# Kernel tuning notes

Measured on AMD Instinct MI355X. Metric: run time of the kernel, lower is better.

Reference implementation:

```python
import jax, jax.numpy as jnp
import numpy as np

N_NODES = 50000
N_EDGES = 600000
LATENT = 128
STEPS = 4
BN_EPS = 1e-5


def _bn(h, gamma, beta):
    # BatchNorm1d in training mode: batch statistics over the row dim (biased var)
    mean = jnp.mean(h, axis=0)
    var = jnp.var(h, axis=0)
    return gamma * (h - mean) * jax.lax.rsqrt(var + BN_EPS) + beta


def setup_inputs() -> dict:
    key = jax.random.key(0)
    ks = jax.random.split(key, 9)
    L, S = LATENT, STEPS
    d = {}
    d["x"] = jax.random.normal(ks[0], (N_NODES, L), dtype=jnp.float32)
    d["edge_attr"] = jax.random.normal(ks[1], (N_EDGES, L), dtype=jnp.float32)
    d["edge_index"] = jax.random.randint(ks[2], (2, N_EDGES), 0, N_NODES, dtype=jnp.int64)
    # MLP weights: small init (BN normalizes hidden activations anyway)
    d["edge_W1"] = jax.random.normal(ks[3], (S, 3 * L, L), dtype=jnp.float32) * (1.0 / np.sqrt(3 * L))
    d["edge_b1"] = jnp.zeros((S, L), jnp.float32)
    d["edge_g1"] = jnp.ones((S, L), jnp.float32)
    d["edge_be1"] = jnp.zeros((S, L), jnp.float32)
    d["edge_W2"] = jax.random.normal(ks[4], (S, L, L), dtype=jnp.float32) * (1.0 / np.sqrt(L))
    d["edge_b2"] = jnp.zeros((S, L), jnp.float32)
    d["node_W1"] = jax.random.normal(ks[5], (S, 2 * L, L), dtype=jnp.float32) * (1.0 / np.sqrt(2 * L))
    d["node_b1"] = jnp.zeros((S, L), jnp.float32)
    d["node_g1"] = jnp.ones((S, L), jnp.float32)
    d["node_be1"] = jnp.zeros((S, L), jnp.float32)
    d["node_W2"] = jax.random.normal(ks[6], (S, L, L), dtype=jnp.float32) * (1.0 / np.sqrt(L))
    d["node_b2"] = jnp.zeros((S, L), jnp.float32)
    return d


def reference(x, edge_attr, edge_index, edge_W1, edge_b1, edge_g1, edge_be1,
              edge_W2, edge_b2, node_W1, node_b1, node_g1, node_be1,
              node_W2, node_b2):
    src = edge_index[0]  # x_j (source)
    dst = edge_index[1]  # x_i (target), also the scatter target
    for s in range(STEPS):
        # --- edge update (message) ---
        m = jnp.concatenate([x[dst], x[src], edge_attr], axis=1)  # [E, 3L]
        h = _bn(m @ edge_W1[s] + edge_b1[s], edge_g1[s], edge_be1[s])
        h = jax.nn.relu(h)
        h = jax.nn.relu(h @ edge_W2[s] + edge_b2[s])
        edge_attr = h + edge_attr  # residual
        # --- aggregate: scatter-sum to target nodes ---
        agg = jax.ops.segment_sum(edge_attr, dst, num_segments=N_NODES)  # [N, L]
        # --- node update ---
        n = jnp.concatenate([x, agg], axis=1)  # [N, 2L]
        h = _bn(n @ node_W1[s] + node_b1[s], node_g1[s], node_be1[s])
        h = jax.nn.relu(h)
        h = jax.nn.relu(h @ node_W2[s] + node_b2[s])
        x = h + x  # residual
    return x, edge_attr
```

## Files before the change

kernel.cpp:

```cpp
#include <hip/hip_runtime.h>
#include <hip/hip_bf16.h>
#include <cstdint>
#include <cstddef>

#define E_N 600000
#define NND 50000
#define L 128
#define EGRID 4688
#define PBLK 16384

typedef unsigned short u16;
typedef unsigned int u32;
typedef __attribute__((ext_vector_type(8))) short bf16x8;
typedef __attribute__((ext_vector_type(4))) float f32x4;

static __device__ __forceinline__ u16 f2bf(float f) {
  union { float f; u32 u; } c; c.f = f;
  return (u16)((c.u + 0x7fffu + ((c.u >> 16) & 1u)) >> 16);
}
static __device__ __forceinline__ u32 pk2(float a, float b) {
  return (u32)f2bf(a) | ((u32)f2bf(b) << 16);
}
static __device__ __forceinline__ float bf2f(u32 h) {
  union { u32 u; float f; } c; c.u = (h & 0xffffu) << 16; return c.f;
}
static __device__ __forceinline__ void atomAddF(float* p, float v) {
#if defined(__HIP_DEVICE_COMPILE__)
  unsafeAtomicAdd(p, v);
#else
  atomicAdd(p, v);
#endif
}
static __device__ __forceinline__ bf16x8 bnrelu8(bf16x8 raw, float4 sca, float4 scb,
                                                 float4 sha, float4 shb) {
  union { bf16x8 v; u16 h[8]; } in; in.v = raw;
  const float sc[8] = {sca.x, sca.y, sca.z, sca.w, scb.x, scb.y, scb.z, scb.w};
  const float sh[8] = {sha.x, sha.y, sha.z, sha.w, shb.x, shb.y, shb.z, shb.w};
  float f[8];
  #pragma unroll
  for (int i = 0; i < 8; ++i) f[i] = fmaxf(bf2f(in.h[i]) * sc[i] + sh[i], 0.f);
  union { bf16x8 v; u32 w[4]; } r;
  #pragma unroll
  for (int i = 0; i < 4; ++i) r.w[i] = pk2(f[2 * i], f[2 * i + 1]);
  return r.v;
}

#define MFMA(a, bfr, c) __builtin_amdgcn_mfma_f32_16x16x32_bf16((a), (bfr), (c), 0, 0, 0)

static __device__ __forceinline__ size_t paddr(int row, int panel, int incol) {
  return (size_t)(row >> 7) * PBLK + (size_t)panel * 2048 + (size_t)(row & 127) * 16 + incol;
}

__global__ __launch_bounds__(256) void k_cvt4(const float* __restrict__ in,
                                              u16* __restrict__ out, int n4) {
  const int i = blockIdx.x * 256 + threadIdx.x;
  if (i < n4) {
    const float4 v = *(const float4*)(in + (size_t)i * 4);
    uint2 o; o.x = pk2(v.x, v.y); o.y = pk2(v.z, v.w);
    *(uint2*)(out + (size_t)i * 4) = o;
  }
}

__global__ __launch_bounds__(256) void k_cvtperm(const float* __restrict__ in_ea,
                                                 const int* __restrict__ perm,
                                                 u16* __restrict__ ea16) {
  const int i = blockIdx.x * 256 + threadIdx.x;
  const int row = i >> 4, part = i & 15;
  if (row < E_N) {
    const float* p = in_ea + (size_t)perm[row] * L + part * 8;
    const float4 f0 = *(const float4*)p, f1 = *(const float4*)(p + 4);
    union { bf16x8 v; u32 w[4]; } r;
    r.w[0] = pk2(f0.x, f0.y); r.w[1] = pk2(f0.z, f0.w);
    r.w[2] = pk2(f1.x, f1.y); r.w[3] = pk2(f1.z, f1.w);
    *(bf16x8*)(ea16 + paddr(row, part >> 1, (part & 1) * 8)) = r.v;
  }
}

__global__ void k_wt(const float* __restrict__ W, u16* __restrict__ Wt, int K) {
  const int idx = blockIdx.x * 256 + threadIdx.x;
  const int total = 4 * K * 128;
  if (idx >= total) return;
  const int s = idx / (K * 128);
  const int rem = idx - s * K * 128;
  const int n = rem / K;
  const int k = rem - n * K;
  Wt[idx] = f2bf(W[(size_t)s * K * 128 + (size_t)k * 128 + n]);
}

__global__ void k_hist(const int* __restrict__ dstI, int* __restrict__ cnt) {
  const int i = blockIdx.x * 256 + threadIdx.x;
  if (i < E_N) atomicAdd(&cnt[dstI[i]], 1);
}

__global__ __launch_bounds__(1024) void k_scan(const int* __restrict__ cnt, int* __restrict__ startA) {
  __shared__ int buf[1024];
  __shared__ int carry;
  const int tid = threadIdx.x;
  if (tid == 0) carry = 0;
  __syncthreads();
  for (int base = 0; base < NND; base += 1024) {
    int v = (base + tid < NND) ? cnt[base + tid] : 0;
    buf[tid] = v;
    __syncthreads();
    for (int off = 1; off < 1024; off <<= 1) {
      int t = (tid >= off) ? buf[tid - off] : 0;
      __syncthreads();
      buf[tid] += t;
      __syncthreads();
    }
    const int incl = buf[tid];
    const int c = carry;
    if (base + tid < NND) startA[base + tid] = c + incl - v;
    __syncthreads();
    if (tid == 1023) carry = c + incl;
    __syncthreads();
  }
  if (tid == 0) startA[NND] = carry;
}

__global__ void k_fill(const int* __restrict__ dstI, const int* __restrict__ startA,
                       int* __restrict__ cur, int* __restrict__ eids) {
  const int i = blockIdx.x * 256 + threadIdx.x;
  if (i < E_N) {
    const int d = dstI[i];
    const int pos = atomicAdd(&cur[d], 1);
    eids[startA[d] + pos] = i;
  }
}

__global__ void k_perm(const int* __restrict__ srcI, const int* __restrict__ dstI,
                       const int* __restrict__ perm,
                       int* __restrict__ srcP, int* __restrict__ dstP) {
  const int i = blockIdx.x * 256 + threadIdx.x;
  if (i < E_N) {
    const int e = perm[i];
    srcP[i] = srcI[e];
    dstP[i] = dstI[e];
  }
}

__global__ __launch_bounds__(256) void k_agg(const u16* __restrict__ ea16,
                                             const int* __restrict__ startA,
                                             u16* __restrict__ agg16) {
  const int node = blockIdx.x * 4 + (threadIdx.x >> 6);
  const int lane = threadIdx.x & 63;
  if (node >= NND) return;
  const int s = startA[node], e = startA[node + 1];
  const size_t poff = (size_t)(lane >> 3) * 2048 + (size_t)((lane & 7) * 2);
  float a0 = 0.f, a1 = 0.f, b0 = 0.f, b1 = 0.f;
  int i = s;
  for (; i + 1 < e; i += 2) {
    const u32 v0 = *(const u32*)(ea16 + (size_t)(i >> 7) * PBLK + (size_t)(i & 127) * 16 + poff);
    const int j = i + 1;
    const u32 v1 = *(const u32*)(ea16 + (size_t)(j >> 7) * PBLK + (size_t)(j & 127) * 16 + poff);
    a0 += bf2f(v0); a1 += bf2f(v0 >> 16);
    b0 += bf2f(v1); b1 += bf2f(v1 >> 16);
  }
  if (i < e) {
    const u32 v = *(const u32*)(ea16 + (size_t)(i >> 7) * PBLK + (size_t)(i & 127) * 16 + poff);
    a0 += bf2f(v); a1 += bf2f(v >> 16);
  }
  *(u32*)(agg16 + (size_t)node * L + lane * 2) = pk2(a0 + b0, a1 + b1);
}

__global__ void k_bnfin(const float* __restrict__ gS, const float* __restrict__ g,
                        const float* __restrict__ be, float invM, float* __restrict__ ss) {
  const int c = threadIdx.x;
  float s1 = 0.f, s2 = 0.f;
  for (int j = 0; j < 64; ++j) { s1 += gS[j * L + c]; s2 += gS[64 * L + j * L + c]; }
  const float mean = s1 * invM;
  const float var = s2 * invM - mean * mean;
  const float sc = g[c] * rsqrtf(var + 1e-5f);
  ss[c] = sc;
  ss[L + c] = be[c] - mean * sc;
}

__global__ __launch_bounds__(512, 4) void k_edge_l1(
    const u16* __restrict__ x16, const u16* __restrict__ ea16,
    const int* __restrict__ srcP, const int* __restrict__ dstP,
    const u16* __restrict__ Wt, const float* __restrict__ b,
    u16* __restrict__ h1, float* __restrict__ gS)
{
  __shared__ __align__(16) char Ws2[2 * 16384];
  __shared__ float red[256];
  const int tid = threadIdx.x, bid = blockIdx.x, row0 = bid * 128;
  const int lane = tid & 63, wid = tid >> 6;
  const int wr = wid >> 1, wc = wid & 1;
  const int l15 = lane & 15, lq = lane >> 4;
  if (tid < 256) red[tid] = 0.f;

  int crw[2], dI[2], sI[2];
  #pragma unroll
  for (int m = 0; m < 2; ++m) {
    crw[m] = min(row0 + wr * 32 + m * 16 + l15, E_N - 1);
    dI[m] = dstP[crw[m]];
    sI[m] = srcP[crw[m]];
  }

  bf16x8 af3[3][2][2];
  auto loadA = [&](int cc, bf16x8 (&dst)[2][2]) {
    #pragma unroll
    for (int m = 0; m < 2; ++m) {
      if (cc < 4) {
        const int node = (cc < 2) ? dI[m] : sI[m];
        const u16* p = x16 + (size_t)node * L + (cc & 1) * 64 + lq * 8;
        dst[m][0] = *(const bf16x8*)p;
        dst[m][1] = *(const bf16x8*)(p + 32);
      } else {
        const int pc = cc - 4;
        dst[m][0] = *(const bf16x8*)(ea16 + paddr(crw[m], pc * 4 + (lq >> 1), (lq & 1) * 8));
        dst[m][1] = *(const bf16x8*)(ea16 + paddr(crw[m], pc * 4 + 2 + (lq >> 1), (lq & 1) * 8));
      }
    }
  };
  loadA(0, af3[0]); loadA(1, af3[1]); loadA(2, af3[2]);

  const int n0 = tid >> 3,         kq0 = (tid & 7) ^ (n0 & 7);
  const int n1 = (tid + 512) >> 3, kq1 = ((tid + 512) & 7) ^ (n1 & 7);
  uint4 wa, wb;
  auto wload = [&](int cc) {
    wa = *(const uint4*)(Wt + (size_t)n0 * 384 + cc * 64 + kq0 * 8);
    wb = *(const uint4*)(Wt + (size_t)n1 * 384 + cc * 64 + kq1 * 8);
  };
  auto wwrite = [&](int buf) {
    *(uint4*)(Ws2 + buf * 16384 + tid * 16) = wa;
    *(uint4*)(Ws2 + buf * 16384 + tid * 16 + 8192) = wb;
  };

  wload(0);
  wwrite(0);
  __syncthreads();

  f32x4 acc[2][4];
  #pragma unroll
  for (int m = 0; m < 2; ++m)
    #pragma unroll
    for (int n = 0; n < 4; ++n) acc[m][n] = (f32x4){0.f, 0.f, 0.f, 0.f};

  #pragma unroll
  for (int cc = 0; cc < 6; ++cc) {
    if (cc + 1 < 6) wload(cc + 1);
    const char* base = Ws2 + (cc & 1) * 16384;
    const bf16x8 (&af)[2][2] = af3[cc % 3];
    #pragma unroll
    for (int k2 = 0; k2 < 2; ++k2)
      #pragma unroll
      for (int n = 0; n < 4; ++n) {
        const int ncol = wc * 64 + n * 16 + l15;
        const int sw = (ncol & 7) << 4;
        const bf16x8 wf = *(const bf16x8*)(base + ((ncol * 128 + k2 * 64 + lq * 16) ^ sw));
        acc[0][n] = MFMA(wf, af[0][k2], acc[0][n]);
        acc[1][n] = MFMA(wf, af[1][k2], acc[1][n]);
      }
    if (cc + 3 < 6) loadA(cc + 3, af3[cc % 3]);
    if (cc + 1 < 6) wwrite((cc + 1) & 1);
    __syncthreads();
  }

  #pragma unroll
  for (int m = 0; m < 2; ++m) {
    const int rl = wr * 32 + m * 16 + l15;
    const bool valid = row0 + rl < E_N;
    #pragma unroll
    for (int n = 0; n < 4; ++n) {
      const int colb = wc * 64 + n * 16 + lq * 4;
      const float4 bb = *(const float4*)(b + colb);
      float o[4], s1[4], s2[4];
      o[0] = acc[m][n][0] + bb.x; o[1] = acc[m][n][1] + bb.y;
      o[2] = acc[m][n][2] + bb.z; o[3] = acc[m][n][3] + bb.w;
      #pragma unroll
      for (int r = 0; r < 4; ++r) {
        s1[r] = valid ? o[r] : 0.f;
        s2[r] = valid ? o[r] * o[r] : 0.f;
      }
      if (valid) {
        ushort4 st;
        st.x = f2bf(o[0]); st.y = f2bf(o[1]); st.z = f2bf(o[2]); st.w = f2bf(o[3]);
        *(ushort4*)(h1 + (size_t)bid * PBLK + (size_t)(wc * 4 + n) * 2048 + rl * 16 + lq * 4) = st;
      }
      #pragma unroll
      for (int off = 1; off < 16; off <<= 1)
        #pragma unroll
        for (int r = 0; r < 4; ++r) {
          s1[r] += __shfl_xor(s1[r], off);
          s2[r] += __shfl_xor(s2[r], off);
        }
      if (l15 == 0) {
        #pragma unroll
        for (int r = 0; r < 4; ++r) {
          atomAddF(&red[colb + r], s1[r]);
          atomAddF(&red[128 + colb + r], s2[r]);
        }
      }
    }
  }
  __syncthreads();
  const int slot = (bid & 63) * L;
  if (tid < 128) atomAddF(&gS[slot + tid], red[tid]);
  else if (tid < 256) atomAddF(&gS[64 * L + slot + (tid - 128)], red[tid]);
}

template <bool WF32>
__global__ __launch_bounds__(512, 4) void k_edge_l2(
    const u16* __restrict__ h1, const float* __restrict__ ss,
    const u16* __restrict__ Wt, const float* __restrict__ b,
    const int* __restrict__ perm,
    float* __restrict__ ea_out, u16* __restrict__ ea16)
{
  __shared__ __align__(16) char Ws2[2 * 16384];
  const int tid = threadIdx.x, bid = blockIdx.x, row0 = bid * 128;
  const int lane = tid & 63, wid = tid >> 6;
  const int wr = wid >> 1, wc = wid & 1;
  const int l15 = lane & 15, lq = lane >> 4;

  int crw[2];
  #pragma unroll
  for (int m = 0; m < 2; ++m)
    crw[m] = min(row0 + wr * 32 + m * 16 + l15, E_N - 1);

  const int n0 = tid >> 3,         kq0 = (tid & 7) ^ (n0 & 7);
  const int n1 = (tid + 512) >> 3, kq1 = ((tid + 512) & 7) ^ (n1 & 7);
  #pragma unroll
  for (int cc = 0; cc < 2; ++cc) {
    const uint4 wa = *(const uint4*)(Wt + (size_t)n0 * 128 + cc * 64 + kq0 * 8);
    const uint4 wb = *(const uint4*)(Wt + (size_t)n1 * 128 + cc * 64 + kq1 * 8);
    *(uint4*)(Ws2 + cc * 16384 + tid * 16) = wa;
    *(uint4*)(Ws2 + cc * 16384 + tid * 16 + 8192) = wb;
  }

  bf16x8 ah[2][2][2];
  #pragma unroll
  for (int cc = 0; cc < 2; ++cc)
    #pragma unroll
    for (int m = 0; m < 2; ++m)
      #pragma unroll
      for (int k2 = 0; k2 < 2; ++k2)
        ah[cc][m][k2] = *(const bf16x8*)(h1 + paddr(crw[m], cc * 4 + k2 * 2 + (lq >> 1), (lq & 1) * 8));
  __syncthreads();

  f32x4 acc[2][4];
  #pragma unroll
  for (int m = 0; m < 2; ++m)
    #pragma unroll
    for (int n = 0; n < 4; ++n) acc[m][n] = (f32x4){0.f, 0.f, 0.f, 0.f};

  #pragma unroll
  for (int cc = 0; cc < 2; ++cc)
    #pragma unroll
    for (int k2 = 0; k2 < 2; ++k2) {
      const int kb = cc * 64 + k2 * 32 + lq * 8;
      const float4 sca = *(const float4*)(ss + kb), scb = *(const float4*)(ss + kb + 4);
      const float4 sha = *(const float4*)(ss + 128 + kb), shb = *(const float4*)(ss + 128 + kb + 4);
      const bf16x8 a0 = bnrelu8(ah[cc][0][k2], sca, scb, sha, shb);
      const bf16x8 a1 = bnrelu8(ah[cc][1][k2], sca, scb, sha, shb);
      const char* base = Ws2 + cc * 16384;
      #pragma unroll
      for (int n = 0; n < 4; ++n) {
        const int ncol = wc * 64 + n * 16 + l15;
        const int sw = (ncol & 7) << 4;
        const bf16x8 wf = *(const bf16x8*)(base + ((ncol * 128 + k2 * 64 + lq * 16) ^ sw));
        acc[0][n] = MFMA(wf, a0, acc[0][n]);
        acc[1][n] = MFMA(wf, a1, acc[1][n]);
      }
    }

  #pragma unroll
  for (int m = 0; m < 2; ++m) {
    const int rl = wr * 32 + m * 16 + l15;
    const int row = row0 + rl;
    if (row < E_N) {
      const int prow = WF32 ? perm[row] : 0;
      #pragma unroll
      for (int n = 0; n < 4; ++n) {
        const int colb = wc * 64 + n * 16 + lq * 4;
        const float4 bb = *(const float4*)(b + colb);
        float o[4];
        o[0] = fmaxf(acc[m][n][0] + bb.x, 0.f);
        o[1] = fmaxf(acc[m][n][1] + bb.y, 0.f);
        o[2] = fmaxf(acc[m][n][2] + bb.z, 0.f);
        o[3] = fmaxf(acc[m][n][3] + bb.w, 0.f);
        u16* ep = ea16 + (size_t)bid * PBLK + (size_t)(wc * 4 + n) * 2048 + rl * 16 + lq * 4;
        const ushort4 rv = *(const ushort4*)ep;
        o[0] += bf2f(rv.x); o[1] += bf2f(rv.y); o[2] += bf2f(rv.z); o[3] += bf2f(rv.w);
        ushort4 st;
        st.x = f2bf(o[0]); st.y = f2bf(o[1]); st.z = f2bf(o[2]); st.w = f2bf(o[3]);
        *(ushort4*)ep = st;
        if (WF32) {
          float4 fv; fv.x = o[0]; fv.y = o[1]; fv.z = o[2]; fv.w = o[3];
          *(float4*)(ea_out + (size_t)prow * L + colb) = fv;
        }
      }
    }
  }
}

__global__ __launch_bounds__(256) void k_node_l1(
    const u16* __restrict__ x16, const u16* __restrict__ agg16,
    const u16* __restrict__ Wt, const float* __restrict__ b,
    u16* __restrict__ h1, float* __restrict__ gS)
{
  __shared__ __align__(16) char Bs[2][16384];
  __shared__ float red[256];
  const int tid = threadIdx.x, bid = blockIdx.x, row0 = bid * 64;
  red[tid] = 0.f;
  const int lane = tid & 63, wid = tid >> 6, wr = wid >> 1, wc = wid & 1;
  const int l15 = lane & 15, lq = lane >> 4;
  const int r0 = row0 + wr * 32 + l15, r1 = r0 + 16;
  const int rr0 = min(r0, NND - 1), rr1 = min(r1, NND - 1);

  const u16* aP[2][2];
  aP[0][0] = x16 + (size_t)rr0 * L;   aP[1][0] = x16 + (size_t)rr1 * L;
  aP[0][1] = agg16 + (size_t)rr0 * L; aP[1][1] = agg16 + (size_t)rr1 * L;

  f32x4 acc[2][4];
  #pragma unroll
  for (int m = 0; m < 2; ++m)
    #pragma unroll
    for (int n = 0; n < 4; ++n) acc[m][n] = (f32x4){0.f, 0.f, 0.f, 0.f};

  auto loadA = [&](int c, bf16x8 (&af)[2][2]) {
    const int seg = c >> 1;
    const int base = (c & 1) * 64 + lq * 8;
    #pragma unroll
    for (int k2 = 0; k2 < 2; ++k2) {
      af[0][k2] = *(const bf16x8*)(aP[0][seg] + base + k2 * 32);
      af[1][k2] = *(const bf16x8*)(aP[1][seg] + base + k2 * 32);
    }
  };
  auto stage = [&](int c, int buf) {
    #pragma unroll
    for (int i = 0; i < 4; ++i) {
      const int slot = tid + i * 256;
      const int n = slot >> 3, kq = slot & 7;
      const uint4 v = *(const uint4*)(Wt + (size_t)n * 256 + c * 64 + kq * 8);
      *(uint4*)(&Bs[buf][0] + ((n * 128 + kq * 16) ^ ((n & 7) << 4))) = v;
    }
  };

  bf16x8 aCur[2][2], aNxt[2][2];
  loadA(0, aCur);
  stage(0, 0);
  __syncthreads();
  #pragma unroll
  for (int c = 0; c < 4; ++c) {
    if (c + 1 < 4) loadA(c + 1, aNxt);
    {
      const char* base = &Bs[c & 1][0];
      #pragma unroll
      for (int k2 = 0; k2 < 2; ++k2)
        #pragma unroll
        for (int n = 0; n < 4; ++n) {
          const int ncol = wc * 64 + n * 16 + l15;
          const bf16x8 bfr = *(const bf16x8*)(base + ((ncol * 128 + k2 * 64 + lq * 16) ^ ((ncol & 7) << 4)));
          acc[0][n] = MFMA(aCur[0][k2], bfr, acc[0][n]);
          acc[1][n] = MFMA(aCur[1][k2], bfr, acc[1][n]);
        }
    }
    if (c + 1 < 4) stage(c + 1, (c + 1) & 1);
    __syncthreads();
    #pragma unroll
    for (int m = 0; m < 2; ++m)
      #pragma unroll
      for (int k2 = 0; k2 < 2; ++k2) aCur[m][k2] = aNxt[m][k2];
  }

  float bb[4], s1[4], s2[4];
  #pragma unroll
  for (int n = 0; n < 4; ++n) { bb[n] = b[wc * 64 + n * 16 + l15]; s1[n] = 0.f; s2[n] = 0.f; }
  #pragma unroll
  for (int m = 0; m < 2; ++m)
    #pragma unroll
    for (int n = 0; n < 4; ++n) {
      const int ncol = wc * 64 + n * 16 + l15;
      #pragma unroll
      for (int r = 0; r < 4; ++r) {
        const int row = row0 + wr * 32 + m * 16 + lq * 4 + r;
        if (row < NND) {
          const float o = acc[m][n][r] + bb[n];
          s1[n] += o; s2[n] += o * o;
          h1[(size_t)row * L + ncol] = f2bf(o);
        }
      }
    }
  #pragma unroll
  for (int n = 0; n < 4; ++n) {
    const int ncol = wc * 64 + n * 16 + l15;
    atomAddF(&red[ncol], s1[n]);
    atomAddF(&red[128 + ncol], s2[n]);
  }
  __syncthreads();
  const int slot = (bid & 63) * L;
  if (tid < 128) atomAddF(&gS[slot + tid], red[tid]);
  else atomAddF(&gS[64 * L + slot + (tid - 128)], red[tid]);
}

__global__ __launch_bounds__(256) void k_node_l2(
    const u16* __restrict__ h1, const float* __restrict__ ss,
    const u16* __restrict__ Wt, const float* __restrict__ b,
    const float* __restrict__ resid, float* __restrict__ x_out,
    u16* __restrict__ x16)
{
  __shared__ __align__(16) char Bs[2][16384];
  const int tid = threadIdx.x, bid = blockIdx.x, row0 = bid * 64;
  const int lane = tid & 63, wid = tid >> 6, wr = wid >> 1, wc = wid & 1;
  const int l15 = lane & 15, lq = lane >> 4;
  const int r0 = row0 + wr * 32 + l15, r1 = r0 + 16;
  const int rr0 = min(r0, NND - 1), rr1 = min(r1, NND - 1);
  const u16* a0 = h1 + (size_t)rr0 * L + lq * 8;
  const u16* a1 = h1 + (size_t)rr1 * L + lq * 8;

  f32x4 acc[2][4];
  #pragma unroll
  for (int m = 0; m < 2; ++m)
    #pragma unroll
    for (int n = 0; n < 4; ++n) acc[m][n] = (f32x4){0.f, 0.f, 0.f, 0.f};

  auto stage = [&](int c, int buf) {
    #pragma unroll
    for (int i = 0; i < 4; ++i) {
      const int slot = tid + i * 256;
      const int n = slot >> 3, kq = slot & 7;
      const uint4 v = *(const uint4*)(Wt + (size_t)n * 128 + c * 64 + kq * 8);
      *(uint4*)(&Bs[buf][0] + ((n * 128 + kq * 16) ^ ((n & 7) << 4))) = v;
    }
  };
  stage(0, 0);
  stage(1, 1);
  bf16x8 raw[2][2][2];
  #pragma unroll
  for (int c = 0; c < 2; ++c)
    #pragma unroll
    for (int k2 = 0; k2 < 2; ++k2) {
      raw[c][0][k2] = *(const bf16x8*)(a0 + c * 64 + k2 * 32);
      raw[c][1][k2] = *(const bf16x8*)(a1 + c * 64 + k2 * 32);
    }
  __syncthreads();

  #pragma unroll
  for (int c = 0; c < 2; ++c) {
    bf16x8 af[2][2];
    #pragma unroll
    for (int k2 = 0; k2 < 2; ++k2) {
      const int kg = c * 64 + k2 * 32 + lq * 8;
      const float4 sca = *(const float4*)(ss + kg), scb = *(const float4*)(ss + kg + 4);
      const float4 sha = *(const float4*)(ss + 128 + kg), shb = *(const float4*)(ss + 128 + kg + 4);
      af[0][k2] = bnrelu8(raw[c][0][k2], sca, scb, sha, shb);
      af[1][k2] = bnrelu8(raw[c][1][k2], sca, scb, sha, shb);
    }
    const char* base = &Bs[c][0];
    #pragma unroll
    for (int k2 = 0; k2 < 2; ++k2)
      #pragma unroll
      for (int n = 0; n < 4; ++n) {
        const int ncol = wc * 64 + n * 16 + l15;
        const bf16x8 bfr = *(const bf16x8*)(base + ((ncol * 128 + k2 * 64 + lq * 16) ^ ((ncol & 7) << 4)));
        acc[0][n] = MFMA(af[0][k2], bfr, acc[0][n]);
        acc[1][n] = MFMA(af[1][k2], bfr, acc[1][n]);
      }
  }

  float bb[4];
  #pragma unroll
  for (int n = 0; n < 4; ++n) bb[n] = b[wc * 64 + n * 16 + l15];
  #pragma unroll
  for (int m = 0; m < 2; ++m)
    #pragma unroll
    for (int n = 0; n < 4; ++n) {
      const int ncol = wc * 64 + n * 16 + l15;
      #pragma unroll
      for (int r = 0; r < 4; ++r) {
        const int row = row0 + wr * 32 + m * 16 + lq * 4 + r;
        if (row < NND) {
          const float o = fmaxf(acc[m][n][r] + bb[n], 0.f) + resid[(size_t)row * L + ncol];
          x_out[(size_t)row * L + ncol] = o;
          x16[(size_t)row * L + ncol] = f2bf(o);
        }
      }
    }
}

extern "C" void kernel_launch(void* const* d_in, const int* in_sizes, int n_in,
                              void* d_out, int out_size, void* d_ws, size_t ws_size,
                              hipStream_t stream) {
  (void)in_sizes; (void)n_in; (void)out_size; (void)ws_size;
  const float* in_x  = (const float*)d_in[0];
  const float* in_ea = (const float*)d_in[1];
  const int*   ei    = (const int*)d_in[2];
  const float* eW1 = (const float*)d_in[3];
  const float* eb1 = (const float*)d_in[4];
  const float* eg1 = (const float*)d_in[5];
  const float* ebe1= (const float*)d_in[6];
  const float* eW2 = (const float*)d_in[7];
  const float* eb2 = (const float*)d_in[8];
  const float* nW1 = (const float*)d_in[9];
  const float* nb1 = (const float*)d_in[10];
  const float* ng1 = (const float*)d_in[11];
  const float* nbe1= (const float*)d_in[12];
  const float* nW2 = (const float*)d_in[13];
  const float* nb2 = (const float*)d_in[14];

  float* x  = (float*)d_out;
  float* ea = (float*)d_out + (size_t)NND * L;

  char* w = (char*)d_ws;
  u16* h1e   = (u16*)w;   w += (size_t)EGRID * PBLK * sizeof(u16);
  u16* ea16  = (u16*)w;   w += (size_t)EGRID * PBLK * sizeof(u16);
  u16* h1n   = (u16*)w;   w += (size_t)NND * L * sizeof(u16);
  u16* x16   = (u16*)w;   w += (size_t)NND * L * sizeof(u16);
  u16* agg16 = (u16*)w;   w += (size_t)NND * L * sizeof(u16);
  float* gS  = (float*)w; w += (size_t)2 * 64 * L * sizeof(float);
  float* ss  = (float*)w; w += 4096;
  u16* eW1t = (u16*)w;   w += (size_t)4 * 128 * 384 * sizeof(u16);
  u16* eW2t = (u16*)w;   w += (size_t)4 * 128 * 128 * sizeof(u16);
  u16* nW1t = (u16*)w;   w += (size_t)4 * 128 * 256 * sizeof(u16);
  u16* nW2t = (u16*)w;   w += (size_t)4 * 128 * 128 * sizeof(u16);
  int* cnt    = (int*)w; w += (size_t)NND * sizeof(int);
  int* cur    = (int*)w; w += (size_t)NND * sizeof(int);
  int* startA = (int*)w; w += (size_t)(NND + 64) * sizeof(int);
  int* eids   = (int*)w; w += (size_t)E_N * sizeof(int);
  int* srcP   = (int*)w; w += (size_t)E_N * sizeof(int);
  int* dstP   = (int*)w; w += (size_t)E_N * sizeof(int);

  const int* srcI = ei;
  const int* dstI = ei + E_N;

  k_cvt4<<<(NND * L / 4 + 255) / 256, 256, 0, stream>>>(in_x, x16, NND * L / 4);
  k_wt<<<(4 * 384 * 128 + 255) / 256, 256, 0, stream>>>(eW1, eW1t, 384);
  k_wt<<<(4 * 128 * 128 + 255) / 256, 256, 0, stream>>>(eW2, eW2t, 128);
  k_wt<<<(4 * 256 * 128 + 255) / 256, 256, 0, stream>>>(nW1, nW1t, 256);
  k_wt<<<(4 * 128 * 128 + 255) / 256, 256, 0, stream>>>(nW2, nW2t, 128);
  hipMemsetAsync(cnt, 0, (size_t)NND * sizeof(int), stream);
  hipMemsetAsync(cur, 0, (size_t)NND * sizeof(int), stream);
  k_hist<<<(E_N + 255) / 256, 256, 0, stream>>>(dstI, cnt);
  k_scan<<<1, 1024, 0, stream>>>(cnt, startA);
  k_fill<<<(E_N + 255) / 256, 256, 0, stream>>>(dstI, startA, cur, eids);
  k_perm<<<(E_N + 255) / 256, 256, 0, stream>>>(srcI, dstI, eids, srcP, dstP);
  k_cvtperm<<<(E_N * 16 + 255) / 256, 256, 0, stream>>>(in_ea, eids, ea16);

  const int ngrid = (NND + 63) / 64;

  for (int s = 0; s < 4; ++s) {
    hipMemsetAsync(gS, 0, (size_t)2 * 64 * L * sizeof(float), stream);
    k_edge_l1<<<EGRID, 512, 0, stream>>>(x16, ea16, srcP, dstP,
        eW1t + (size_t)s * 128 * 384, eb1 + (size_t)s * L, h1e, gS);
    k_bnfin<<<1, 128, 0, stream>>>(gS, eg1 + (size_t)s * L, ebe1 + (size_t)s * L,
        1.f / (float)E_N, ss);
    if (s < 3)
      k_edge_l2<false><<<EGRID, 512, 0, stream>>>(h1e, ss,
          eW2t + (size_t)s * 128 * 128, eb2 + (size_t)s * L, eids, ea, ea16);
    else
      k_edge_l2<true><<<EGRID, 512, 0, stream>>>(h1e, ss,
          eW2t + (size_t)s * 128 * 128, eb2 + (size_t)s * L, eids, ea, ea16);
    k_agg<<<(NND + 3) / 4, 256, 0, stream>>>(ea16, startA, agg16);
    hipMemsetAsync(gS, 0, (size_t)2 * 64 * L * sizeof(float), stream);
    k_node_l1<<<ngrid, 256, 0, stream>>>(x16, agg16,
        nW1t + (size_t)s * 128 * 256, nb1 + (size_t)s * L, h1n, gS);
    k_bnfin<<<1, 128, 0, stream>>>(gS, ng1 + (size_t)s * L, nbe1 + (size_t)s * L,
        1.f / (float)NND, ss);
    k_node_l2<<<ngrid, 256, 0, stream>>>(h1n, ss,
        nW2t + (size_t)s * 128 * 128, nb2 + (size_t)s * L,
        (s == 0) ? in_x : x, x, x16);
  }
}
```

Before: 2.005 ms.

## Remap edge block IDs per XCD, widen BN stat slots, merge shuffle reductions

```diff
diff --git a/kernel.cpp b/kernel.cpp
--- a/kernel.cpp
+++ b/kernel.cpp
@@ -7,7 +7,9 @@
 #define NND 50000
 #define L 128
 #define EGRID 4688
+#define XCHUNK 586
 #define PBLK 16384
+#define NSLOT 256
 
 typedef unsigned short u16;
 typedef unsigned int u32;
@@ -167,7 +169,7 @@
                         const float* __restrict__ be, float invM, float* __restrict__ ss) {
   const int c = threadIdx.x;
   float s1 = 0.f, s2 = 0.f;
-  for (int j = 0; j < 64; ++j) { s1 += gS[j * L + c]; s2 += gS[64 * L + j * L + c]; }
+  for (int j = 0; j < NSLOT; ++j) { s1 += gS[j * L + c]; s2 += gS[NSLOT * L + j * L + c]; }
   const float mean = s1 * invM;
   const float var = s2 * invM - mean * mean;
   const float sc = g[c] * rsqrtf(var + 1e-5f);
@@ -183,7 +185,9 @@
 {
   __shared__ __align__(16) char Ws2[2 * 16384];
   __shared__ float red[256];
-  const int tid = threadIdx.x, bid = blockIdx.x, row0 = bid * 128;
+  const int tid = threadIdx.x;
+  const int bid = (blockIdx.x & 7) * XCHUNK + (blockIdx.x >> 3);
+  const int row0 = bid * 128;
   const int lane = tid & 63, wid = tid >> 6;
   const int wr = wid >> 1, wc = wid & 1;
   const int l15 = lane & 15, lq = lane >> 4;
@@ -258,46 +262,44 @@
   }
 
   #pragma unroll
-  for (int m = 0; m < 2; ++m) {
-    const int rl = wr * 32 + m * 16 + l15;
-    const bool valid = row0 + rl < E_N;
-    #pragma unroll
-    for (int n = 0; n < 4; ++n) {
-      const int colb = wc * 64 + n * 16 + lq * 4;
-      const float4 bb = *(const float4*)(b + colb);
-      float o[4], s1[4], s2[4];
+  for (int n = 0; n < 4; ++n) {
+    const int colb = wc * 64 + n * 16 + lq * 4;
+    const float4 bb = *(const float4*)(b + colb);
+    float s1[4] = {0.f, 0.f, 0.f, 0.f}, s2[4] = {0.f, 0.f, 0.f, 0.f};
+    #pragma unroll
+    for (int m = 0; m < 2; ++m) {
+      const int rl = wr * 32 + m * 16 + l15;
+      const bool valid = row0 + rl < E_N;
+      float o[4];
       o[0] = acc[m][n][0] + bb.x; o[1] = acc[m][n][1] + bb.y;
       o[2] = acc[m][n][2] + bb.z; o[3] = acc[m][n][3] + bb.w;
-      #pragma unroll
-      for (int r = 0; r < 4; ++r) {
-        s1[r] = valid ? o[r] : 0.f;
-        s2[r] = valid ? o[r] * o[r] : 0.f;
-      }
       if (valid) {
+        #pragma unroll
+        for (int r = 0; r < 4; ++r) { s1[r] += o[r]; s2[r] += o[r] * o[r]; }
         ushort4 st;
         st.x = f2bf(o[0]); st.y = f2bf(o[1]); st.z = f2bf(o[2]); st.w = f2bf(o[3]);
         *(ushort4*)(h1 + (size_t)bid * PBLK + (size_t)(wc * 4 + n) * 2048 + rl * 16 + lq * 4) = st;
       }
-      #pragma unroll
-      for (int off = 1; off < 16; off <<= 1)
-        #pragma unroll
-        for (int r = 0; r < 4; ++r) {
-          s1[r] += __shfl_xor(s1[r], off);
-          s2[r] += __shfl_xor(s2[r], off);
-        }
-      if (l15 == 0) {
-        #pragma unroll
-        for (int r = 0; r < 4; ++r) {
-          atomAddF(&red[colb + r], s1[r]);
-          atomAddF(&red[128 + colb + r], s2[r]);
-        }
+    }
+    #pragma unroll
+    for (int off = 1; off < 16; off <<= 1)
+      #pragma unroll
+      for (int r = 0; r < 4; ++r) {
+        s1[r] += __shfl_xor(s1[r], off);
+        s2[r] += __shfl_xor(s2[r], off);
+      }
+    if (l15 == 0) {
+      #pragma unroll
+      for (int r = 0; r < 4; ++r) {
+        atomAddF(&red[colb + r], s1[r]);
+        atomAddF(&red[128 + colb + r], s2[r]);
       }
     }
   }
   __syncthreads();
-  const int slot = (bid & 63) * L;
+  const int slot = (bid & (NSLOT - 1)) * L;
   if (tid < 128) atomAddF(&gS[slot + tid], red[tid]);
-  else if (tid < 256) atomAddF(&gS[64 * L + slot + (tid - 128)], red[tid]);
+  else if (tid < 256) atomAddF(&gS[NSLOT * L + slot + (tid - 128)], red[tid]);
 }
 
 template <bool WF32>
@@ -308,7 +310,9 @@
     float* __restrict__ ea_out, u16* __restrict__ ea16)
 {
   __shared__ __align__(16) char Ws2[2 * 16384];
-  const int tid = threadIdx.x, bid = blockIdx.x, row0 = bid * 128;
+  const int tid = threadIdx.x;
+  const int bid = (blockIdx.x & 7) * XCHUNK + (blockIdx.x >> 3);
+  const int row0 = bid * 128;
   const int lane = tid & 63, wid = tid >> 6;
   const int wr = wid >> 1, wc = wid & 1;
   const int l15 = lane & 15, lq = lane >> 4;
@@ -489,9 +493,9 @@
     atomAddF(&red[128 + ncol], s2[n]);
   }
   __syncthreads();
-  const int slot = (bid & 63) * L;
+  const int slot = (bid & (NSLOT - 1)) * L;
   if (tid < 128) atomAddF(&gS[slot + tid], red[tid]);
-  else atomAddF(&gS[64 * L + slot + (tid - 128)], red[tid]);
+  else atomAddF(&gS[NSLOT * L + slot + (tid - 128)], red[tid]);
 }
 
 __global__ __launch_bounds__(256) void k_node_l2(
@@ -608,7 +612,7 @@
   u16* h1n   = (u16*)w;   w += (size_t)NND * L * sizeof(u16);
   u16* x16   = (u16*)w;   w += (size_t)NND * L * sizeof(u16);
   u16* agg16 = (u16*)w;   w += (size_t)NND * L * sizeof(u16);
-  float* gS  = (float*)w; w += (size_t)2 * 64 * L * sizeof(float);
+  float* gS  = (float*)w; w += (size_t)2 * NSLOT * L * sizeof(float);
   float* ss  = (float*)w; w += 4096;
   u16* eW1t = (u16*)w;   w += (size_t)4 * 128 * 384 * sizeof(u16);
   u16* eW2t = (u16*)w;   w += (size_t)4 * 128 * 128 * sizeof(u16);
@@ -640,7 +644,7 @@
   const int ngrid = (NND + 63) / 64;
 
   for (int s = 0; s < 4; ++s) {
-    hipMemsetAsync(gS, 0, (size_t)2 * 64 * L * sizeof(float), stream);
+    hipMemsetAsync(gS, 0, (size_t)2 * NSLOT * L * sizeof(float), stream);
     k_edge_l1<<<EGRID, 512, 0, stream>>>(x16, ea16, srcP, dstP,
         eW1t + (size_t)s * 128 * 384, eb1 + (size_t)s * L, h1e, gS);
     k_bnfin<<<1, 128, 0, stream>>>(gS, eg1 + (size_t)s * L, ebe1 + (size_t)s * L,
@@ -652,7 +656,7 @@
       k_edge_l2<true><<<EGRID, 512, 0, stream>>>(h1e, ss,
           eW2t + (size_t)s * 128 * 128, eb2 + (size_t)s * L, eids, ea, ea16);
     k_agg<<<(NND + 3) / 4, 256, 0, stream>>>(ea16, startA, agg16);
-    hipMemsetAsync(gS, 0, (size_t)2 * 64 * L * sizeof(float), stream);
+    hipMemsetAsync(gS, 0, (size_t)2 * NSLOT * L * sizeof(float), stream);
     k_node_l1<<<ngrid, 256, 0, stream>>>(x16, agg16,
         nW1t + (size_t)s * 128 * 256, nb1 + (size_t)s * L, h1n, gS);
     k_bnfin<<<1, 128, 0, stream>>>(gS, ng1 + (size_t)s * L, nbe1 + (size_t)s * L,
```

New measurement: 1.944 ms. 1.03x faster.
